# Kernel tuning notes

Hardware: AMD Instinct MI355X
Metric: run time of the kernel (lower is better)

## Reference

```python
import jax, jax.numpy as jnp
import numpy as np

D_MODEL = 512
N_HEADS = 8
B, T = 2, 2048
EPS = 1e-6


def _phi(x):
    # ELU feature map: elu(x) + 1 (always positive)
    return jax.nn.elu(x) + 1.0


def setup_inputs() -> dict:
    key = jax.random.key(0)
    ks = jax.random.split(key, 9)
    s = 1.0 / np.sqrt(D_MODEL)
    x = jax.random.normal(ks[0], (B, T, D_MODEL), dtype=jnp.float32)
    Wq = jax.random.uniform(ks[1], (D_MODEL, D_MODEL), jnp.float32, -s, s)
    bq = jax.random.uniform(ks[2], (D_MODEL,), jnp.float32, -s, s)
    Wk = jax.random.uniform(ks[3], (D_MODEL, D_MODEL), jnp.float32, -s, s)
    bk = jax.random.uniform(ks[4], (D_MODEL,), jnp.float32, -s, s)
    Wv = jax.random.uniform(ks[5], (D_MODEL, D_MODEL), jnp.float32, -s, s)
    bv = jax.random.uniform(ks[6], (D_MODEL,), jnp.float32, -s, s)
    Wo = jax.random.uniform(ks[7], (D_MODEL, D_MODEL), jnp.float32, -s, s)
    bo = jax.random.uniform(ks[8], (D_MODEL,), jnp.float32, -s, s)
    return {"x": x, "Wq": Wq, "bq": bq, "Wk": Wk, "bk": bk,
            "Wv": Wv, "bv": bv, "Wo": Wo, "bo": bo}


def reference(x, Wq, bq, Wk, bk, Wv, bv, Wo, bo):
    Bb, Tt, _ = x.shape
    H = N_HEADS
    D = D_MODEL // H

    def heads(W, b):
        # (B,T,d_model) -> (B,H,T,D)
        return (x @ W + b).reshape(Bb, Tt, H, D).transpose(0, 2, 1, 3)

    Q = _phi(heads(Wq, bq))
    K = _phi(heads(Wk, bk))
    V = heads(Wv, bv)

    # Causal linear attention: S_t = sum_{j<=t} phi(K_j) ⊗ V_j, z_t = sum_{j<=t} phi(K_j)
    KV = jnp.einsum('bhtd,bhtm->bhtdm', K, V)   # (B,H,T,D,D)
    S = jnp.cumsum(KV, axis=2)
    z = jnp.cumsum(K, axis=2)
    num = jnp.einsum('bhtd,bhtdm->bhtm', Q, S)  # (B,H,T,D)
    den = jnp.maximum(jnp.einsum('bhtd,bhtd->bht', Q, z), EPS)[..., None]
    out = num / den

    out = out.transpose(0, 2, 1, 3).reshape(Bb, Tt, D_MODEL)
    return out @ Wo + bo
```

## Files before the change

### kernel.cpp

```cpp
#include <hip/hip_runtime.h>
#include <math.h>

#define DM 512
#define NH 8
#define HD 64
#define BB 2
#define TT 2048
#define CHUNK 64
#define NC (TT / CHUNK)
#define BH (BB * NH)
#define ROWS (BB * TT)
#define EPSV 1e-6f

typedef short bf16x8 __attribute__((ext_vector_type(8)));
typedef float f32x4 __attribute__((ext_vector_type(4)));
typedef unsigned short us;

union U4 { us h[4]; uint2 u; };

__device__ __forceinline__ us f2bf(float f) {
    unsigned int u = __float_as_uint(f);
    return (us)((u + 0x7FFFu + ((u >> 16) & 1u)) >> 16);
}
__device__ __forceinline__ float bf2f(us h) {
    return __uint_as_float(((unsigned int)h) << 16);
}
__device__ __forceinline__ void gload16(const void* g, void* l) {
    __builtin_amdgcn_global_load_lds(
        (const __attribute__((address_space(1))) unsigned int*)g,
        (__attribute__((address_space(3))) unsigned int*)l, 16, 0, 0);
}
#define SWZ(r, k) ((k) ^ (((r) & 7) << 3))

__global__ __launch_bounds__(256) void prep(
    const float* __restrict__ x,
    const float* __restrict__ Wq, const float* __restrict__ Wk,
    const float* __restrict__ Wv, const float* __restrict__ Wo,
    us* __restrict__ xb, us* __restrict__ WT)
{
    const int bid = blockIdx.x, tid = threadIdx.x;
    __shared__ float tl[32][33];
    if (bid < 2048) {
        const int i = bid * 256 + tid;
        float4 v = ((const float4*)x)[i];
        U4 o;
        o.h[0] = f2bf(v.x); o.h[1] = f2bf(v.y);
        o.h[2] = f2bf(v.z); o.h[3] = f2bf(v.w);
        ((uint2*)xb)[i] = o.u;
    } else {
        const int b2 = bid - 2048;
        const int which = b2 >> 8, t = b2 & 255;
        const float* W = (which == 0) ? Wq : (which == 1) ? Wk : (which == 2) ? Wv : Wo;
        us* O = WT + (size_t)which * DM * DM;
        const int r0 = (t >> 4) * 32, c0 = (t & 15) * 32;
        const int tr = tid >> 3, tc = tid & 7;
        float4 v = *(const float4*)&W[(size_t)(r0 + tr) * DM + c0 + tc * 4];
        tl[tr][tc * 4 + 0] = v.x; tl[tr][tc * 4 + 1] = v.y;
        tl[tr][tc * 4 + 2] = v.z; tl[tr][tc * 4 + 3] = v.w;
        __syncthreads();
        U4 o;
#pragma unroll
        for (int i = 0; i < 4; ++i) o.h[i] = f2bf(tl[tc * 4 + i][tr]);
        *(uint2*)&O[(size_t)(c0 + tr) * DM + r0 + tc * 4] = o.u;
    }
}

__device__ __forceinline__ void stage_tiles(
    const us* __restrict__ Ag, const us* __restrict__ Bg,
    int r0, int c0, int k0, int tid, us* As, us* Bs)
{
    const int fa = tid * 8;
#pragma unroll
    for (int i = 0; i < 2; ++i) {
        const int f = fa + i * 2048, row = f >> 6, kp = f & 63;
        gload16(Ag + (size_t)(r0 + row) * DM + k0 + SWZ(row, kp), As + f);
    }
#pragma unroll
    for (int i = 0; i < 4; ++i) {
        const int f = fa + i * 2048, row = f >> 6, kp = f & 63;
        gload16(Bg + (size_t)(c0 + row) * DM + k0 + SWZ(row, kp), Bs + f);
    }
}

__device__ __forceinline__ void gemm64x128(
    const us* __restrict__ Ag, const us* __restrict__ Bg,
    int r0, int c0, int tid, us* Asl, us* Bsl, f32x4 (&acc)[2][4])
{
    const int lane = tid & 63, wid = tid >> 6;
    const int wr = wid >> 1, wc = wid & 1;
    const int lrow = lane & 15, lk8 = (lane >> 4) * 8;

    stage_tiles(Ag, Bg, r0, c0, 0, tid, Asl, Bsl);
    __syncthreads();
    int cur = 0;
    for (int k0 = 0; k0 < DM; k0 += 64) {
        if (k0 + 64 < DM)
            stage_tiles(Ag, Bg, r0, c0, k0 + 64, tid,
                        Asl + (cur ^ 1) * 4096, Bsl + (cur ^ 1) * 8192);
        const us* As = Asl + cur * 4096;
        const us* Bs = Bsl + cur * 8192;
#pragma unroll
        for (int kin = 0; kin < 64; kin += 32) {
            bf16x8 af[2], bfr[4];
#pragma unroll
            for (int mi = 0; mi < 2; ++mi) {
                const int row = wr * 32 + mi * 16 + lrow;
                af[mi] = *(const bf16x8*)&As[row * 64 + SWZ(row, kin + lk8)];
            }
#pragma unroll
            for (int ni = 0; ni < 4; ++ni) {
                const int row = wc * 64 + ni * 16 + lrow;
                bfr[ni] = *(const bf16x8*)&Bs[row * 64 + SWZ(row, kin + lk8)];
            }
#pragma unroll
            for (int mi = 0; mi < 2; ++mi)
#pragma unroll
                for (int ni = 0; ni < 4; ++ni)
                    acc[mi][ni] = __builtin_amdgcn_mfma_f32_16x16x32_bf16(
                        af[mi], bfr[ni], acc[mi][ni], 0, 0, 0);
        }
        __syncthreads();
        cur ^= 1;
    }
}

__global__ __launch_bounds__(256) void qkv_mfma(
    const us* __restrict__ xb, const us* __restrict__ WT,
    const float* __restrict__ bq, const float* __restrict__ bk,
    const float* __restrict__ bv,
    us* __restrict__ qn, us* __restrict__ kn,
    us* __restrict__ kt, us* __restrict__ vt)
{
    const int which = blockIdx.z;
    const us* Bg = WT + (size_t)which * DM * DM;
    const float* bias = (which == 0) ? bq : (which == 1) ? bk : bv;

    __shared__ us sh[24576];
    us* Asl = sh;
    us* Bsl = sh + 8192;

    f32x4 acc[2][4] = {};
    const int r0 = blockIdx.x * 64, c0 = blockIdx.y * 128;
    const int tid = threadIdx.x;

    gemm64x128(xb, Bg, r0, c0, tid, Asl, Bsl, acc);

    const int lane = tid & 63, wid = tid >> 6;
    const int wr = wid >> 1, wc = wid & 1;
    const int lrow = lane & 15, lr4 = (lane >> 4) * 4;
    const int b = r0 >> 11, t0b = r0 & (TT - 1);

    if (which == 0) {
#pragma unroll
        for (int mi = 0; mi < 2; ++mi) {
            const int t0g = t0b + wr * 32 + mi * 16 + lr4;
#pragma unroll
            for (int ni = 0; ni < 4; ++ni) {
                const int col = c0 + wc * 64 + ni * 16 + lrow;
                const int h = col >> 6, d = col & 63;
                const float bc = bias[col];
#pragma unroll
                for (int r = 0; r < 4; ++r) {
                    float y = acc[mi][ni][r] + bc;
                    y = (y > 0.f) ? (y + 1.f) : __expf(y);
                    qn[((size_t)(b * NH + h) * TT + t0g + r) * HD + d] = f2bf(y);
                }
            }
        }
        return;
    }

    us* Cb = sh;
#pragma unroll
    for (int mi = 0; mi < 2; ++mi) {
        const int tL = wr * 32 + mi * 16 + lr4;
#pragma unroll
        for (int ni = 0; ni < 4; ++ni) {
            const int colL = wc * 64 + ni * 16 + lrow;
            const int col = c0 + colL;
            const float bc = bias[col];
            U4 p4;
#pragma unroll
            for (int r = 0; r < 4; ++r) {
                float y = acc[mi][ni][r] + bc;
                if (which == 1) y = (y > 0.f) ? (y + 1.f) : __expf(y);
                p4.h[r] = f2bf(y);
            }
            if (which == 1) {
                const int h = col >> 6, d = col & 63;
#pragma unroll
                for (int r = 0; r < 4; ++r)
                    kn[((size_t)(b * NH + h) * TT + t0b + tL + r) * HD + d] = p4.h[r];
            }
            *(uint2*)&Cb[colL * 72 + tL] = p4.u;
        }
    }
    __syncthreads();

    us* dst = (which == 1) ? kt : vt;
#pragma unroll
    for (int it = 0; it < 4; ++it) {
        const int colL = it * 32 + wid * 8 + (lane >> 3);
        const int tch = (lane & 7) * 8;
        const uint4 v = *(const uint4*)&Cb[colL * 72 + tch];
        const int col = c0 + colL, h = col >> 6, d = col & 63;
        *(uint4*)&dst[((size_t)(b * NH + h) * HD + d) * TT + t0b + tch] = v;
    }
}

__global__ __launch_bounds__(256) void out_mfma(
    const us* __restrict__ Ag, const us* __restrict__ WoT,
    const float* __restrict__ bias, float* __restrict__ out)
{
    __shared__ us Asl[2 * 4096];
    __shared__ us Bsl[2 * 8192];
    f32x4 acc[2][4] = {};
    const int r0 = blockIdx.x * 64, c0 = blockIdx.y * 128;
    const int tid = threadIdx.x;

    gemm64x128(Ag, WoT, r0, c0, tid, Asl, Bsl, acc);

    const int lane = tid & 63, wid = tid >> 6;
    const int wr = wid >> 1, wc = wid & 1;
    const int lrow = lane & 15, lr4 = (lane >> 4) * 4;

#pragma unroll
    for (int mi = 0; mi < 2; ++mi)
#pragma unroll
        for (int ni = 0; ni < 4; ++ni) {
            const int col = c0 + wc * 64 + ni * 16 + lrow;
            const float bc = bias[col];
#pragma unroll
            for (int r = 0; r < 4; ++r) {
                const int row = r0 + wr * 32 + mi * 16 + lr4 + r;
                out[(size_t)row * DM + col] = acc[mi][ni][r] + bc;
            }
        }
}

__global__ __launch_bounds__(256) void chunk_sums(
    const us* __restrict__ kt, const us* __restrict__ vt,
    us* __restrict__ kvc, float* __restrict__ zc)
{
    const int blk = blockIdx.x, bh = blk >> 5, c = blk & 31;
    const int t0 = c * CHUNK;
    __shared__ us Ksl[4096], Vsl[4096];
    __shared__ float partial[4][64];
    const int tid = threadIdx.x;
    const us* ktb = kt + (size_t)bh * HD * TT;
    const us* vtb = vt + (size_t)bh * HD * TT;

#pragma unroll
    for (int i = 0; i < 2; ++i) {
        const int f = tid * 8 + i * 2048, row = f >> 6, kp = f & 63;
        const int kl = SWZ(row, kp);
        gload16(ktb + (size_t)row * TT + t0 + kl, Ksl + f);
        gload16(vtb + (size_t)row * TT + t0 + kl, Vsl + f);
    }
    __syncthreads();

    const int lane = tid & 63, wid = tid >> 6;
    const int wr = wid >> 1, wc = wid & 1;
    const int lrow = lane & 15, lk8 = (lane >> 4) * 8, lr4 = (lane >> 4) * 4;

    f32x4 acc[2][2] = {};
#pragma unroll
    for (int kin = 0; kin < 64; kin += 32) {
        bf16x8 af[2], bfr[2];
#pragma unroll
        for (int mi = 0; mi < 2; ++mi) {
            const int row = wr * 32 + mi * 16 + lrow;
            af[mi] = *(const bf16x8*)&Vsl[row * 64 + SWZ(row, kin + lk8)];
        }
#pragma unroll
        for (int ni = 0; ni < 2; ++ni) {
            const int row = wc * 32 + ni * 16 + lrow;
            bfr[ni] = *(const bf16x8*)&Ksl[row * 64 + SWZ(row, kin + lk8)];
        }
#pragma unroll
        for (int mi = 0; mi < 2; ++mi)
#pragma unroll
            for (int ni = 0; ni < 2; ++ni)
                acc[mi][ni] = __builtin_amdgcn_mfma_f32_16x16x32_bf16(
                    af[mi], bfr[ni], acc[mi][ni], 0, 0, 0);
    }

    us* dst = kvc + (size_t)blk * 4096;
#pragma unroll
    for (int mi = 0; mi < 2; ++mi)
#pragma unroll
        for (int ni = 0; ni < 2; ++ni) {
            const int d2 = wr * 32 + mi * 16 + lr4;
            const int d1 = wc * 32 + ni * 16 + lrow;
#pragma unroll
            for (int r = 0; r < 4; ++r)
                dst[(d2 + r) * 64 + d1] = f2bf(acc[mi][ni][r]);
        }

    {
        const int p = tid >> 6, d = tid & 63;
        float s = 0.f;
#pragma unroll
        for (int j = 0; j < 16; ++j)
            s += bf2f(Ksl[d * 64 + SWZ(d, p * 16 + j)]);
        partial[p][d] = s;
    }
    __syncthreads();
    if (tid < 64)
        zc[(size_t)blk * 64 + tid] =
            partial[0][tid] + partial[1][tid] + partial[2][tid] + partial[3][tid];
}

__global__ __launch_bounds__(256) void scan(
    const us* __restrict__ kvc, const float* __restrict__ zc,
    us* __restrict__ spr, float* __restrict__ zpr)
{
    const int bh = blockIdx.x, seg = blockIdx.y, tid = threadIdx.x;
    if (seg < 8) {
        const int e = seg * 512 + tid * 2;
        const size_t base = (size_t)(bh * NC) * 4096 + e;
        unsigned u[NC];
#pragma unroll
        for (int c = 0; c < NC; ++c)
            u[c] = *(const unsigned*)(kvc + base + (size_t)c * 4096);
        float r0 = 0.f, r1 = 0.f;
#pragma unroll
        for (int c = 0; c < NC; ++c) {
            const unsigned p = (unsigned)f2bf(r0) | ((unsigned)f2bf(r1) << 16);
            *(unsigned*)(spr + base + (size_t)c * 4096) = p;
            r0 += bf2f((us)(u[c] & 0xFFFF));
            r1 += bf2f((us)(u[c] >> 16));
        }
    } else if (tid < 64) {
        const size_t base = (size_t)(bh * NC) * 64 + tid;
        float zv[NC];
#pragma unroll
        for (int c = 0; c < NC; ++c) zv[c] = zc[base + (size_t)c * 64];
        float run = 0.f;
#pragma unroll
        for (int c = 0; c < NC; ++c) {
            zpr[base + (size_t)c * 64] = run;
            run += zv[c];
        }
    }
}

__global__ __launch_bounds__(256) void chunk_attn(
    const us* __restrict__ qn, const us* __restrict__ kn,
    const us* __restrict__ vt, const us* __restrict__ spr,
    const float* __restrict__ zpr, us* __restrict__ attn)
{
    const int blk = blockIdx.x, bh = blk >> 5, c = blk & 31;
    const int t0 = c * CHUNK;
    __shared__ us Qs[4096], Kns[4096], Vts[4096], Sts[4096], Abf[4096];
    __shared__ float zp[64], den[64], part[4][64];
    const int tid = threadIdx.x;

    const us* qb = qn + ((size_t)bh * TT + t0) * HD;
    const us* kb = kn + ((size_t)bh * TT + t0) * HD;
    const us* vb = vt + (size_t)bh * HD * TT;
    const us* sb = spr + (size_t)blk * 4096;

#pragma unroll
    for (int i = 0; i < 2; ++i) {
        const int f = tid * 8 + i * 2048, row = f >> 6, kp = f & 63;
        const int kl = SWZ(row, kp);
        gload16(qb + (size_t)row * HD + kl, Qs + f);
        gload16(kb + (size_t)row * HD + kl, Kns + f);
        gload16(vb + (size_t)row * TT + t0 + kl, Vts + f);
        gload16(sb + (size_t)row * 64 + kl, Sts + f);
    }
    if (tid < 64) zp[tid] = zpr[(size_t)blk * 64 + tid];
    __syncthreads();

    const int lane = tid & 63, wid = tid >> 6;
    const int wr = wid >> 1, wc = wid & 1;
    const int lrow = lane & 15, lk8 = (lane >> 4) * 8, lr4 = (lane >> 4) * 4;

    f32x4 accs[2][2] = {};
#pragma unroll
    for (int kin = 0; kin < 64; kin += 32) {
        bf16x8 af[2], bfr[2];
#pragma unroll
        for (int mi = 0; mi < 2; ++mi) {
            const int row = wr * 32 + mi * 16 + lrow;
            af[mi] = *(const bf16x8*)&Qs[row * 64 + SWZ(row, kin + lk8)];
        }
#pragma unroll
        for (int ni = 0; ni < 2; ++ni) {
            const int row = wc * 32 + ni * 16 + lrow;
            bfr[ni] = *(const bf16x8*)&Kns[row * 64 + SWZ(row, kin + lk8)];
        }
#pragma unroll
        for (int mi = 0; mi < 2; ++mi)
#pragma unroll
            for (int ni = 0; ni < 2; ++ni)
                accs[mi][ni] = __builtin_amdgcn_mfma_f32_16x16x32_bf16(
                    af[mi], bfr[ni], accs[mi][ni], 0, 0, 0);
    }

#pragma unroll
    for (int mi = 0; mi < 2; ++mi)
#pragma unroll
        for (int ni = 0; ni < 2; ++ni) {
            const int j = wc * 32 + ni * 16 + lrow;
#pragma unroll
            for (int r = 0; r < 4; ++r) {
                const int i = wr * 32 + mi * 16 + lr4 + r;
                const float v = (j <= i) ? accs[mi][ni][r] : 0.f;
                Abf[i * 64 + SWZ(i, j)] = f2bf(v);
            }
        }
    __syncthreads();

    {
        const int p = tid >> 6, i = tid & 63;
        float s = 0.f;
#pragma unroll
        for (int jj = 0; jj < 16; ++jj) {
            const int j = p * 16 + jj;
            s += bf2f(Abf[i * 64 + SWZ(i, j)]);
            s += bf2f(Qs[i * 64 + SWZ(i, j)]) * zp[j];
        }
        part[p][i] = s;
    }
    __syncthreads();
    if (tid < 64)
        den[tid] = fmaxf(part[0][tid] + part[1][tid] + part[2][tid] + part[3][tid], EPSV);
    __syncthreads();

    f32x4 acco[2][2] = {};
#pragma unroll
    for (int kin = 0; kin < 64; kin += 32) {
        bf16x8 af[2], bfr[2], ag[2], bgr[2];
#pragma unroll
        for (int mi = 0; mi < 2; ++mi) {
            const int row = wr * 32 + mi * 16 + lrow;
            af[mi] = *(const bf16x8*)&Abf[row * 64 + SWZ(row, kin + lk8)];
            ag[mi] = *(const bf16x8*)&Qs[row * 64 + SWZ(row, kin + lk8)];
        }
#pragma unroll
        for (int ni = 0; ni < 2; ++ni) {
            const int row = wc * 32 + ni * 16 + lrow;
            bfr[ni] = *(const bf16x8*)&Vts[row * 64 + SWZ(row, kin + lk8)];
            bgr[ni] = *(const bf16x8*)&Sts[row * 64 + SWZ(row, kin + lk8)];
        }
#pragma unroll
        for (int mi = 0; mi < 2; ++mi)
#pragma unroll
            for (int ni = 0; ni < 2; ++ni) {
                acco[mi][ni] = __builtin_amdgcn_mfma_f32_16x16x32_bf16(
                    af[mi], bfr[ni], acco[mi][ni], 0, 0, 0);
                acco[mi][ni] = __builtin_amdgcn_mfma_f32_16x16x32_bf16(
                    ag[mi], bgr[ni], acco[mi][ni], 0, 0, 0);
            }
    }

    const int b = bh >> 3, h = bh & 7;
#pragma unroll
    for (int mi = 0; mi < 2; ++mi)
#pragma unroll
        for (int ni = 0; ni < 2; ++ni) {
            const int d2 = wc * 32 + ni * 16 + lrow;
#pragma unroll
            for (int r = 0; r < 4; ++r) {
                const int i = wr * 32 + mi * 16 + lr4 + r;
                attn[((size_t)b * TT + t0 + i) * DM + h * HD + d2] =
                    f2bf(acco[mi][ni][r] / den[i]);
            }
        }
}

extern "C" void kernel_launch(void* const* d_in, const int* in_sizes, int n_in,
                              void* d_out, int out_size, void* d_ws, size_t ws_size,
                              hipStream_t stream)
{
    const float* x  = (const float*)d_in[0];
    const float* Wq = (const float*)d_in[1];
    const float* bq = (const float*)d_in[2];
    const float* Wk = (const float*)d_in[3];
    const float* bk = (const float*)d_in[4];
    const float* Wv = (const float*)d_in[5];
    const float* bv = (const float*)d_in[6];
    const float* Wo = (const float*)d_in[7];
    const float* bo = (const float*)d_in[8];
    float* out = (float*)d_out;

    const size_t SZ = (size_t)BH * TT * HD;
    us* xb  = (us*)d_ws;
    us* WT  = xb + SZ;
    us* qn  = WT + (size_t)4 * DM * DM;
    us* kn  = qn + SZ;
    us* kt  = kn + SZ;
    us* vt  = kt + SZ;
    us* kvc = vt + SZ;
    us* spr = kvc + SZ;
    float* zc  = (float*)(spr + SZ);
    float* zpr = zc + (size_t)BH * NC * 64;
    us* attn = xb;

    prep<<<3072, 256, 0, stream>>>(x, Wq, Wk, Wv, Wo, xb, WT);
    qkv_mfma<<<dim3(ROWS / 64, DM / 128, 3), 256, 0, stream>>>(
        xb, WT, bq, bk, bv, qn, kn, kt, vt);
    chunk_sums<<<BH * NC, 256, 0, stream>>>(kt, vt, kvc, zc);
    scan<<<dim3(BH, 9), 256, 0, stream>>>(kvc, zc, spr, zpr);
    chunk_attn<<<BH * NC, 256, 0, stream>>>(qn, kn, vt, spr, zpr, attn);
    out_mfma<<<dim3(ROWS / 64, DM / 128), 256, 0, stream>>>(
        attn, WT + (size_t)3 * DM * DM, bo, out);
}
```

Measured before the change: 46.18 us.

## Fuse chunk prefix scan into attention kernel and coalesce Q/K row stores

Removes the separate scan kernel. Each chunk_attn block now sums the preceding chunks' KV states and z sums itself, which does redundant O(c) work per chunk but saves one launch and the spr/zpr round trip through global memory. The qkv epilogue also stages the Q and K row-major outputs through a swizzled shared tile so they are written with 16-byte coalesced stores instead of scattered 2-byte stores. Later chunks read up to 31 prior 8KB states each, which adds load imbalance and extra memory traffic.

```diff
diff --git a/kernel.cpp b/kernel.cpp
--- a/kernel.cpp
+++ b/kernel.cpp
@@ -17,6 +17,7 @@
 typedef unsigned short us;
 
 union U4 { us h[4]; uint2 u; };
+union U8 { us h[8]; uint4 u; };
 
 __device__ __forceinline__ us f2bf(float f) {
     unsigned int u = __float_as_uint(f);
@@ -31,6 +32,7 @@
         (__attribute__((address_space(3))) unsigned int*)l, 16, 0, 0);
 }
 #define SWZ(r, k) ((k) ^ (((r) & 7) << 3))
+#define SWZT(row, col) ((((((col) >> 3) ^ ((row) & 15)) << 3)) | ((col) & 7))
 
 __global__ __launch_bounds__(256) void prep(
     const float* __restrict__ x,
@@ -150,61 +152,50 @@
     const int lrow = lane & 15, lr4 = (lane >> 4) * 4;
     const int b = r0 >> 11, t0b = r0 & (TT - 1);
 
-    if (which == 0) {
-#pragma unroll
-        for (int mi = 0; mi < 2; ++mi) {
-            const int t0g = t0b + wr * 32 + mi * 16 + lr4;
-#pragma unroll
-            for (int ni = 0; ni < 4; ++ni) {
-                const int col = c0 + wc * 64 + ni * 16 + lrow;
-                const int h = col >> 6, d = col & 63;
-                const float bc = bias[col];
-#pragma unroll
-                for (int r = 0; r < 4; ++r) {
-                    float y = acc[mi][ni][r] + bc;
-                    y = (y > 0.f) ? (y + 1.f) : __expf(y);
-                    qn[((size_t)(b * NH + h) * TT + t0g + r) * HD + d] = f2bf(y);
-                }
-            }
-        }
-        return;
-    }
-
-    us* Cb = sh;
+    us* CbT = sh;
+    us* CbD = sh + 8192;
+
 #pragma unroll
     for (int mi = 0; mi < 2; ++mi) {
         const int tL = wr * 32 + mi * 16 + lr4;
 #pragma unroll
         for (int ni = 0; ni < 4; ++ni) {
             const int colL = wc * 64 + ni * 16 + lrow;
-            const int col = c0 + colL;
-            const float bc = bias[col];
+            const float bc = bias[c0 + colL];
             U4 p4;
 #pragma unroll
             for (int r = 0; r < 4; ++r) {
                 float y = acc[mi][ni][r] + bc;
-                if (which == 1) y = (y > 0.f) ? (y + 1.f) : __expf(y);
+                if (which < 2) y = (y > 0.f) ? (y + 1.f) : __expf(y);
                 p4.h[r] = f2bf(y);
-            }
-            if (which == 1) {
-                const int h = col >> 6, d = col & 63;
-#pragma unroll
-                for (int r = 0; r < 4; ++r)
-                    kn[((size_t)(b * NH + h) * TT + t0b + tL + r) * HD + d] = p4.h[r];
-            }
-            *(uint2*)&Cb[colL * 72 + tL] = p4.u;
-        }
-    }
-    __syncthreads();
-
-    us* dst = (which == 1) ? kt : vt;
-#pragma unroll
-    for (int it = 0; it < 4; ++it) {
-        const int colL = it * 32 + wid * 8 + (lane >> 3);
-        const int tch = (lane & 7) * 8;
-        const uint4 v = *(const uint4*)&Cb[colL * 72 + tch];
-        const int col = c0 + colL, h = col >> 6, d = col & 63;
-        *(uint4*)&dst[((size_t)(b * NH + h) * HD + d) * TT + t0b + tch] = v;
+                if (which < 2) CbT[(tL + r) * 128 + SWZT(tL + r, colL)] = p4.h[r];
+            }
+            if (which >= 1) *(uint2*)&CbD[colL * 72 + tL] = p4.u;
+        }
+    }
+    __syncthreads();
+
+    if (which < 2) {
+        us* dstn = (which == 0) ? qn : kn;
+#pragma unroll
+        for (int it = 0; it < 4; ++it) {
+            const int idx = it * 2048 + tid * 8;
+            const int row = idx >> 7, col = idx & 127;
+            const uint4 v = *(const uint4*)&CbT[row * 128 + SWZT(row, col)];
+            const int h = (c0 + col) >> 6, d = col & 63;
+            *(uint4*)&dstn[((size_t)(b * NH + h) * TT + t0b + row) * HD + d] = v;
+        }
+    }
+    if (which >= 1) {
+        us* dst = (which == 1) ? kt : vt;
+#pragma unroll
+        for (int it = 0; it < 4; ++it) {
+            const int colL = it * 32 + wid * 8 + (lane >> 3);
+            const int tch = (lane & 7) * 8;
+            const uint4 v = *(const uint4*)&CbD[colL * 72 + tch];
+            const int col = c0 + colL, h = col >> 6, d = col & 63;
+            *(uint4*)&dst[((size_t)(b * NH + h) * HD + d) * TT + t0b + tch] = v;
+        }
     }
 }
 
@@ -311,44 +302,10 @@
             partial[0][tid] + partial[1][tid] + partial[2][tid] + partial[3][tid];
 }
 
-__global__ __launch_bounds__(256) void scan(
-    const us* __restrict__ kvc, const float* __restrict__ zc,
-    us* __restrict__ spr, float* __restrict__ zpr)
-{
-    const int bh = blockIdx.x, seg = blockIdx.y, tid = threadIdx.x;
-    if (seg < 8) {
-        const int e = seg * 512 + tid * 2;
-        const size_t base = (size_t)(bh * NC) * 4096 + e;
-        unsigned u[NC];
-#pragma unroll
-        for (int c = 0; c < NC; ++c)
-            u[c] = *(const unsigned*)(kvc + base + (size_t)c * 4096);
-        float r0 = 0.f, r1 = 0.f;
-#pragma unroll
-        for (int c = 0; c < NC; ++c) {
-            const unsigned p = (unsigned)f2bf(r0) | ((unsigned)f2bf(r1) << 16);
-            *(unsigned*)(spr + base + (size_t)c * 4096) = p;
-            r0 += bf2f((us)(u[c] & 0xFFFF));
-            r1 += bf2f((us)(u[c] >> 16));
-        }
-    } else if (tid < 64) {
-        const size_t base = (size_t)(bh * NC) * 64 + tid;
-        float zv[NC];
-#pragma unroll
-        for (int c = 0; c < NC; ++c) zv[c] = zc[base + (size_t)c * 64];
-        float run = 0.f;
-#pragma unroll
-        for (int c = 0; c < NC; ++c) {
-            zpr[base + (size_t)c * 64] = run;
-            run += zv[c];
-        }
-    }
-}
-
 __global__ __launch_bounds__(256) void chunk_attn(
     const us* __restrict__ qn, const us* __restrict__ kn,
-    const us* __restrict__ vt, const us* __restrict__ spr,
-    const float* __restrict__ zpr, us* __restrict__ attn)
+    const us* __restrict__ vt, const us* __restrict__ kvc,
+    const float* __restrict__ zc, us* __restrict__ attn)
 {
     const int blk = blockIdx.x, bh = blk >> 5, c = blk & 31;
     const int t0 = c * CHUNK;
@@ -359,7 +316,6 @@
     const us* qb = qn + ((size_t)bh * TT + t0) * HD;
     const us* kb = kn + ((size_t)bh * TT + t0) * HD;
     const us* vb = vt + (size_t)bh * HD * TT;
-    const us* sb = spr + (size_t)blk * 4096;
 
 #pragma unroll
     for (int i = 0; i < 2; ++i) {
@@ -368,9 +324,27 @@
         gload16(qb + (size_t)row * HD + kl, Qs + f);
         gload16(kb + (size_t)row * HD + kl, Kns + f);
         gload16(vb + (size_t)row * TT + t0 + kl, Vts + f);
-        gload16(sb + (size_t)row * 64 + kl, Sts + f);
-    }
-    if (tid < 64) zp[tid] = zpr[(size_t)blk * 64 + tid];
+    }
+#pragma unroll
+    for (int i = 0; i < 2; ++i) {
+        const int f = tid * 8 + i * 2048, row = f >> 6, kp = f & 63;
+        const us* src = kvc + (size_t)(bh * NC) * 4096 + row * 64 + kp;
+        float sacc[8] = {};
+        for (int s = 0; s < c; ++s) {
+            const bf16x8 v = *(const bf16x8*)(src + (size_t)s * 4096);
+#pragma unroll
+            for (int e = 0; e < 8; ++e) sacc[e] += bf2f((us)v[e]);
+        }
+        U8 p;
+#pragma unroll
+        for (int e = 0; e < 8; ++e) p.h[e] = f2bf(sacc[e]);
+        *(uint4*)&Sts[row * 64 + SWZ(row, kp)] = p.u;
+    }
+    if (tid < 64) {
+        float zv = 0.f;
+        for (int s = 0; s < c; ++s) zv += zc[(size_t)(bh * NC + s) * 64 + tid];
+        zp[tid] = zv;
+    }
     __syncthreads();
 
     const int lane = tid & 63, wid = tid >> 6;
@@ -494,17 +468,14 @@
     us* kt  = kn + SZ;
     us* vt  = kt + SZ;
     us* kvc = vt + SZ;
-    us* spr = kvc + SZ;
-    float* zc  = (float*)(spr + SZ);
-    float* zpr = zc + (size_t)BH * NC * 64;
+    float* zc = (float*)(kvc + SZ);
     us* attn = xb;
 
     prep<<<3072, 256, 0, stream>>>(x, Wq, Wk, Wv, Wo, xb, WT);
     qkv_mfma<<<dim3(ROWS / 64, DM / 128, 3), 256, 0, stream>>>(
         xb, WT, bq, bk, bv, qn, kn, kt, vt);
     chunk_sums<<<BH * NC, 256, 0, stream>>>(kt, vt, kvc, zc);
-    scan<<<dim3(BH, 9), 256, 0, stream>>>(kvc, zc, spr, zpr);
-    chunk_attn<<<BH * NC, 256, 0, stream>>>(qn, kn, vt, spr, zpr, attn);
+    chunk_attn<<<BH * NC, 256, 0, stream>>>(qn, kn, vt, kvc, zc, attn);
     out_mfma<<<dim3(ROWS / 64, DM / 128), 256, 0, stream>>>(
         attn, WT + (size_t)3 * DM * DM, bo, out);
 }
```

Result: slower. 62.85 us (+36.1%).
